# Optimization experiments

Measured on AMD Instinct MI355X. Metric: run time of the kernel, lower is better.

## Reference

```python
import jax, jax.numpy as jnp
import numpy as np

N_NODES = 50000
N_EDGES = 800000
HIDDEN = 128
NUM_RBF = 32
N_GRAPHS = 500
VOCAB = 100


def setup_inputs() -> dict:
    key = jax.random.key(0)
    ks = jax.random.split(key, 16)
    x = jax.random.randint(ks[0], (N_NODES,), 0, VOCAB)
    edge_index = jax.random.randint(ks[1], (2, N_EDGES), 0, N_NODES)
    edge_attr = jax.random.normal(ks[2], (N_EDGES, NUM_RBF), dtype=jnp.float32)
    batch = jnp.sort(jax.random.randint(ks[3], (N_NODES,), 0, N_GRAPHS))
    zdim = 2 * HIDDEN + NUM_RBF
    s = 1.0 / np.sqrt(zdim)
    params = {"emb": jax.random.normal(ks[4], (VOCAB, HIDDEN), dtype=jnp.float32)}
    for l, k0 in zip((1, 2, 3), (5, 8, 11)):
        params[f"Wf{l}"] = jax.random.uniform(ks[k0], (zdim, HIDDEN), minval=-s, maxval=s, dtype=jnp.float32)
        params[f"bf{l}"] = jnp.zeros((HIDDEN,), dtype=jnp.float32)
        params[f"Ws{l}"] = jax.random.uniform(ks[k0 + 1], (zdim, HIDDEN), minval=-s, maxval=s, dtype=jnp.float32)
        params[f"bs{l}"] = jnp.zeros((HIDDEN,), dtype=jnp.float32)
    sl = 1.0 / np.sqrt(HIDDEN)
    params["Wlin"] = jax.random.uniform(ks[14], (HIDDEN, HIDDEN), minval=-sl, maxval=sl, dtype=jnp.float32)
    params["blin"] = jnp.zeros((HIDDEN,), dtype=jnp.float32)
    return {"x": x, "edge_index": edge_index, "edge_attr": edge_attr, "batch": batch, **params}


def _cgconv(h, src, dst, edge_attr, Wf, bf, Ws, bs):
    # z = [x_i || x_j || e_ij]; i = target (dst), j = source (src)
    z = jnp.concatenate([h[dst], h[src], edge_attr], axis=-1)  # [E, 2H+D]
    msg = jax.nn.sigmoid(z @ Wf + bf) * jax.nn.softplus(z @ Ws + bs)  # [E, H]
    agg = jax.ops.segment_sum(msg, dst, num_segments=N_NODES)
    return h + agg


def reference(x, edge_index, edge_attr, batch, emb,
              Wf1, bf1, Ws1, bs1, Wf2, bf2, Ws2, bs2, Wf3, bf3, Ws3, bs3,
              Wlin, blin):
    src, dst = edge_index[0], edge_index[1]
    h = emb[x]  # [N, H]
    h = jax.nn.relu(_cgconv(h, src, dst, edge_attr, Wf1, bf1, Ws1, bs1))
    h = jax.nn.relu(_cgconv(h, src, dst, edge_attr, Wf2, bf2, Ws2, bs2))
    h = jax.nn.relu(_cgconv(h, src, dst, edge_attr, Wf3, bf3, Ws3, bs3))
    sums = jax.ops.segment_sum(h, batch, num_segments=N_GRAPHS)  # [G, H]
    counts = jax.ops.segment_sum(jnp.ones((N_NODES,), h.dtype), batch, num_segments=N_GRAPHS)
    pooled = sums / jnp.maximum(counts, 1.0)[:, None]
    return pooled @ Wlin + blin
```

## Files before the change

### kernel.cpp

```cpp
#include <hip/hip_runtime.h>
#include <hip/hip_bf16.h>
#include <hip/hip_fp16.h>
#include <cstdint>
#include <cstddef>

#define NNODES 50000
#define NEDGES 800000
#define HID 128
#define NRBF 32
#define NGRAPH 500
#define NB_SCAN 196
#define EPB 64
#define NEBLK (NEDGES / EPB)
#define SROWA2 66

typedef __attribute__((ext_vector_type(8))) short short8;
typedef __attribute__((ext_vector_type(4))) float f32x4;

__device__ inline short f2bf(float x) {
  __hip_bfloat16 b = __float2bfloat16(x);
  return *reinterpret_cast<short*>(&b);
}

__device__ inline unsigned int pk_bf16(float a, float b) {
  unsigned int r;
  asm("v_cvt_pk_bf16_f32 %0, %1, %2" : "=v"(r) : "v"(a), "v"(b));
  return r;
}
__device__ inline unsigned int pk_f16(float a, float b) {
  unsigned int r;
  asm("v_cvt_pkrtz_f16_f32 %0, %1, %2" : "=v"(r) : "v"(a), "v"(b));
  return r;
}
__device__ inline unsigned int pk_add_f16(unsigned int a, unsigned int b) {
  unsigned int r;
  asm("v_pk_add_f16 %0, %1, %2" : "=v"(r) : "v"(a), "v"(b));
  return r;
}
__device__ inline float aexp2(float x) {
  float r;
  asm("v_exp_f32 %0, %1" : "=v"(r) : "v"(x));
  return r;
}
__device__ inline float aexp2_nabs(float x) {
  float r;
  asm("v_exp_f32 %0, -abs(%1)" : "=v"(r) : "v"(x));
  return r;
}
__device__ inline float alog2(float x) {
  float r;
  asm("v_log_f32 %0, %1" : "=v"(r) : "v"(x));
  return r;
}

#define SC_F (-1.4426950408889634f)
#define SC_S (1.4426950408889634f)

__global__ void prep_all(
    const float* __restrict__ Wf0, const float* __restrict__ Ws0,
    const float* __restrict__ bf0, const float* __restrict__ bs0,
    const float* __restrict__ Wf1, const float* __restrict__ Ws1,
    const float* __restrict__ bf1, const float* __restrict__ bs1,
    const float* __restrict__ Wf2, const float* __restrict__ Ws2,
    const float* __restrict__ bf2, const float* __restrict__ bs2,
    unsigned short* __restrict__ WtB3, unsigned short* __restrict__ WnB3,
    float* __restrict__ biasv3) {
  const int l = blockIdx.y;
  const float* Wf = (l == 0) ? Wf0 : ((l == 1) ? Wf1 : Wf2);
  const float* Ws = (l == 0) ? Ws0 : ((l == 1) ? Ws1 : Ws2);
  const float* bf = (l == 0) ? bf0 : ((l == 1) ? bf1 : bf2);
  const float* bs = (l == 0) ? bs0 : ((l == 1) ? bs1 : bs2);
  unsigned short* WtB = WtB3 + l * 8192;
  unsigned short* WnB = WnB3 + l * 65536;
  float* biasv = biasv3 + l * 256;

  int i0 = blockIdx.x * blockDim.x + threadIdx.x;
  if (i0 < 8192) {
    int i = i0;
    int j = i & 7, lane = (i >> 3) & 63, t = i >> 9;
    int q = lane >> 4, n = lane & 15;
    int k = q * 8 + j, c = (t & 7) * 16 + n;
    const float* W = (t < 8) ? Wf : Ws;
    const float sc = (t < 8) ? SC_F : SC_S;
    WtB[i] = (unsigned short)f2bf(W[(size_t)(256 + k) * HID + c] * sc);
  } else if (i0 < 8192 + 65536) {
    int i = i0 - 8192;
    int j = i & 7;
    int lane = (i >> 3) & 63;
    int tk = (i >> 9) & 3;
    int tc = i >> 11;
    int q = lane >> 4, n = lane & 15;
    int k = tk * 32 + q * 8 + j;
    float v;
    int which;
    if (tc < 16) {
      int g = tc >> 1;
      which = tc & 1;
      int c = g * 16 + n;
      const float* W = which ? Ws : Wf;
      v = W[(size_t)k * HID + c];
    } else {
      int g = (tc - 16) >> 1;
      which = (tc - 16) & 1;
      int c = g * 16 + n;
      const float* W = which ? Ws : Wf;
      v = W[(size_t)(128 + k) * HID + c];
    }
    WnB[i] = (unsigned short)f2bf(v * (which ? SC_S : SC_F));
    if (i < 256) {
      int c2 = i >> 1, w2 = i & 1;
      biasv[i] = w2 ? bs[c2] * SC_S : bf[c2] * SC_F;
    }
  }
}

__global__ void deg_hist(const int* __restrict__ dst, int* __restrict__ deg) {
  int e = blockIdx.x * blockDim.x + threadIdx.x;
  if (e < NEDGES) atomicAdd(&deg[dst[e]], 1);
}

__global__ __launch_bounds__(256) void scan_block(const int* __restrict__ deg, int* __restrict__ bsum) {
  __shared__ int s[256];
  int i = blockIdx.x * 256 + threadIdx.x;
  s[threadIdx.x] = (i < NNODES) ? deg[i] : 0;
  __syncthreads();
  for (int off = 128; off > 0; off >>= 1) {
    if (threadIdx.x < off) s[threadIdx.x] += s[threadIdx.x + off];
    __syncthreads();
  }
  if (threadIdx.x == 0) bsum[blockIdx.x] = s[0];
}

__global__ __launch_bounds__(256) void scan_top(const int* __restrict__ bsum,
                                                int* __restrict__ bpre) {
  __shared__ int s[256];
  int t = threadIdx.x;
  int v = (t < NB_SCAN) ? bsum[t] : 0;
  s[t] = v;
  __syncthreads();
  for (int off = 1; off < 256; off <<= 1) {
    int u = (t >= off) ? s[t - off] : 0;
    __syncthreads();
    s[t] += u;
    __syncthreads();
  }
  if (t < NB_SCAN) bpre[t] = s[t] - v;
}

__global__ __launch_bounds__(256) void scan_final(const int* __restrict__ deg,
                                                  const int* __restrict__ bpre,
                                                  int* __restrict__ cursor) {
  __shared__ int s[256];
  int i = blockIdx.x * 256 + threadIdx.x;
  int v = (i < NNODES) ? deg[i] : 0;
  s[threadIdx.x] = v;
  __syncthreads();
  for (int off = 1; off < 256; off <<= 1) {
    int t = (threadIdx.x >= off) ? s[threadIdx.x - off] : 0;
    __syncthreads();
    s[threadIdx.x] += t;
    __syncthreads();
  }
  if (i < NNODES) cursor[i] = bpre[blockIdx.x] + s[threadIdx.x] - v;
}

__global__ void scatter_edges_pack(const int* __restrict__ src, const int* __restrict__ dst,
                                   const float* __restrict__ eattr, int* __restrict__ cursor,
                                   int2* __restrict__ se2, unsigned short* __restrict__ eaB) {
  int e = blockIdx.x * blockDim.x + threadIdx.x;
  if (e >= NEDGES) return;
  int d = dst[e];
  int pos = atomicAdd(&cursor[d], 1);
  se2[pos] = make_int2(src[e], d);
  const float* ep = eattr + (size_t)e * NRBF;
  unsigned short* op = eaB + (size_t)pos * NRBF;
#pragma unroll
  for (int part = 0; part < 4; ++part) {
    const float4 v0 = *(const float4*)&ep[part * 8];
    const float4 v1 = *(const float4*)&ep[part * 8 + 4];
    uint4 o;
    o.x = pk_bf16(v0.x, v0.y);
    o.y = pk_bf16(v0.z, v0.w);
    o.z = pk_bf16(v1.x, v1.y);
    o.w = pk_bf16(v1.z, v1.w);
    *(uint4*)&op[part * 8] = o;
  }
}

__global__ __launch_bounds__(256) void node_mfma(
    const int* __restrict__ x, const float* __restrict__ emb,
    float* __restrict__ h, float* __restrict__ agg,
    const unsigned short* __restrict__ WnB, const float* __restrict__ biasv,
    unsigned int* __restrict__ Pdst, unsigned int* __restrict__ Psrc, int mode, int N) {
  const int tid = threadIdx.x;
  const int wv = tid >> 6;
  const int lane = tid & 63;
  const int q = lane >> 4;
  const int n = lane & 15;
  const int nb = blockIdx.x * 32 + (wv >> 1) * 16;
  const int srcwave = wv & 1;
  const int ctile0 = srcwave * 16;

  const bool valid = (nb + n) < N;
  int anode = nb + n;
  if (anode >= N) anode = N - 1;
  float* hp = h + (size_t)anode * HID;

  short8 a[4];
  if (mode == 0) {
    const float* ep = emb + (size_t)x[anode] * HID;
#pragma unroll
    for (int kt = 0; kt < 4; ++kt) {
      const float4 e0 = *(const float4*)&ep[kt * 32 + q * 8];
      const float4 e1 = *(const float4*)&ep[kt * 32 + q * 8 + 4];
      if (valid && !srcwave) {
        *(float4*)&hp[kt * 32 + q * 8] = e0;
        *(float4*)&hp[kt * 32 + q * 8 + 4] = e1;
      }
      union { short8 s8; unsigned int u32[4]; } au;
      au.u32[0] = pk_bf16(e0.x, e0.y);
      au.u32[1] = pk_bf16(e0.z, e0.w);
      au.u32[2] = pk_bf16(e1.x, e1.y);
      au.u32[3] = pk_bf16(e1.z, e1.w);
      a[kt] = au.s8;
    }
  } else {
    float* ap = agg + (size_t)anode * HID;
    float4 ev[8];
#pragma unroll
    for (int kt = 0; kt < 4; ++kt) {
      float4 e0 = *(const float4*)&hp[kt * 32 + q * 8];
      float4 e1 = *(const float4*)&hp[kt * 32 + q * 8 + 4];
      const float4 g0 = *(const float4*)&ap[kt * 32 + q * 8];
      const float4 g1 = *(const float4*)&ap[kt * 32 + q * 8 + 4];
      e0.x = fmaxf(e0.x + g0.x, 0.f); e0.y = fmaxf(e0.y + g0.y, 0.f);
      e0.z = fmaxf(e0.z + g0.z, 0.f); e0.w = fmaxf(e0.w + g0.w, 0.f);
      e1.x = fmaxf(e1.x + g1.x, 0.f); e1.y = fmaxf(e1.y + g1.y, 0.f);
      e1.z = fmaxf(e1.z + g1.z, 0.f); e1.w = fmaxf(e1.w + g1.w, 0.f);
      ev[2 * kt] = e0;
      ev[2 * kt + 1] = e1;
      union { short8 s8; unsigned int u32[4]; } au;
      au.u32[0] = pk_bf16(e0.x, e0.y);
      au.u32[1] = pk_bf16(e0.z, e0.w);
      au.u32[2] = pk_bf16(e1.x, e1.y);
      au.u32[3] = pk_bf16(e1.z, e1.w);
      a[kt] = au.s8;
    }
    __syncthreads();
    if (valid && !srcwave) {
      const float4 z4 = {0.f, 0.f, 0.f, 0.f};
#pragma unroll
      for (int kt = 0; kt < 4; ++kt) {
        *(float4*)&hp[kt * 32 + q * 8] = ev[2 * kt];
        *(float4*)&hp[kt * 32 + q * 8 + 4] = ev[2 * kt + 1];
        *(float4*)&ap[kt * 32 + q * 8] = z4;
        *(float4*)&ap[kt * 32 + q * 8 + 4] = z4;
      }
    }
  }

  const short8* WnB8 = (const short8*)WnB;
  f32x4 acc[16];
#pragma unroll
  for (int tc = 0; tc < 16; ++tc) acc[tc] = (f32x4){0.f, 0.f, 0.f, 0.f};

#pragma unroll
  for (int tc = 0; tc < 16; ++tc) {
#pragma unroll
    for (int kt = 0; kt < 4; ++kt) {
      short8 b = WnB8[((size_t)((ctile0 + tc) * 4 + kt)) * 64 + lane];
      acc[tc] = __builtin_amdgcn_mfma_f32_16x16x32_bf16(a[kt], b, acc[tc], 0, 0, 0);
    }
  }

  if (!srcwave) {
#pragma unroll
    for (int r = 0; r < 4; ++r) {
      const int node = nb + q * 4 + r;
      if (node < N) {
        unsigned int o[8];
#pragma unroll
        for (int g2 = 0; g2 < 8; ++g2) {
          const int c = g2 * 16 + n;
          o[g2] = pk_f16(acc[2 * g2][r] + biasv[2 * c], acc[2 * g2 + 1][r] + biasv[2 * c + 1]);
        }
        *(uint4*)&Pdst[(size_t)node * 128 + n * 8] = make_uint4(o[0], o[1], o[2], o[3]);
        *(uint4*)&Pdst[(size_t)node * 128 + n * 8 + 4] = make_uint4(o[4], o[5], o[6], o[7]);
      }
    }
  } else {
#pragma unroll
    for (int r = 0; r < 4; ++r) {
      const int node = nb + q * 4 + r;
      if (node < N) {
        unsigned int o[8];
#pragma unroll
        for (int g2 = 0; g2 < 8; ++g2) {
          o[g2] = pk_f16(acc[2 * g2][r], acc[2 * g2 + 1][r]);
        }
        *(uint4*)&Psrc[(size_t)node * 128 + n * 8] = make_uint4(o[0], o[1], o[2], o[3]);
        *(uint4*)&Psrc[(size_t)node * 128 + n * 8 + 4] = make_uint4(o[4], o[5], o[6], o[7]);
      }
    }
  }
}

__global__ __launch_bounds__(256) void edge_mfma(
    const unsigned int* __restrict__ Pdst, const unsigned int* __restrict__ Psrc,
    const unsigned short* __restrict__ eaB, const unsigned short* __restrict__ WtB,
    const int2* __restrict__ se2, float* __restrict__ agg) {
  __shared__ unsigned int actL[EPB * SROWA2];
  __shared__ int dstL[EPB];
  __shared__ int grpStart[EPB + 1];
  __shared__ int sndS;

  const int tid = threadIdx.x;
  const int base = blockIdx.x * EPB;
  const int lane = tid & 63;
  const int wv = tid >> 6;
  const int q = lane >> 4;
  const int n = lane & 15;
  const int rowb = wv * 16 + q * 4;

  if (tid < EPB) {
    int2 sd = se2[base + tid];
    dstL[tid] = sd.y;
    int d = sd.y;
    int dprev = __shfl_up(d, 1);
    int flag = (tid == 0 || dprev != d) ? 1 : 0;
    unsigned long long mask = __ballot(flag);
    unsigned long long below = (lane == 63) ? ~0ull : ((1ull << (lane + 1)) - 1);
    int slot = __popcll(mask & below) - 1;
    if (flag) grpStart[slot] = tid;
    if (tid == 0) {
      int nd = __popcll(mask);
      sndS = nd;
      grpStart[nd] = EPB;
    }
  }

  const short8 afrag = *(const short8*)&eaB[(size_t)(base + wv * 16 + n) * 32 + q * 8];

  uint4 spd[8];
#pragma unroll
  for (int r = 0; r < 4; ++r) {
    const int2 sd = se2[base + rowb + r];
    const uint4* ps4 = (const uint4*)(Psrc + (size_t)sd.x * 128 + n * 8);
    const uint4* pd4 = (const uint4*)(Pdst + (size_t)sd.y * 128 + n * 8);
    const uint4 s0 = ps4[0], s1 = ps4[1];
    const uint4 d0 = pd4[0], d1 = pd4[1];
    spd[r * 2].x = pk_add_f16(s0.x, d0.x);
    spd[r * 2].y = pk_add_f16(s0.y, d0.y);
    spd[r * 2].z = pk_add_f16(s0.z, d0.z);
    spd[r * 2].w = pk_add_f16(s0.w, d0.w);
    spd[r * 2 + 1].x = pk_add_f16(s1.x, d1.x);
    spd[r * 2 + 1].y = pk_add_f16(s1.y, d1.y);
    spd[r * 2 + 1].z = pk_add_f16(s1.z, d1.z);
    spd[r * 2 + 1].w = pk_add_f16(s1.w, d1.w);
  }

  const short8* WtB8 = (const short8*)WtB;
  float va[4][4];
#pragma unroll
  for (int t = 0; t < 8; ++t) {
    f32x4 cinf, cins;
#pragma unroll
    for (int r = 0; r < 4; ++r) {
      const uint4 v = spd[r * 2 + (t >> 2)];
      const unsigned int sv = ((t & 3) == 0) ? v.x : ((t & 3) == 1) ? v.y
                             : ((t & 3) == 2) ? v.z : v.w;
      const float2 pz = __half22float2(*reinterpret_cast<const __half2*>(&sv));
      cinf[r] = pz.x;
      cins[r] = pz.y;
    }
    short8 bfr = WtB8[t * 64 + lane];
    short8 bsr = WtB8[(8 + t) * 64 + lane];
    f32x4 cf = __builtin_amdgcn_mfma_f32_16x16x32_bf16(afrag, bfr, cinf, 0, 0, 0);
    f32x4 cs = __builtin_amdgcn_mfma_f32_16x16x32_bf16(afrag, bsr, cins, 0, 0, 0);
#pragma unroll
    for (int r = 0; r < 4; ++r) {
      const float sig = __builtin_amdgcn_rcpf(1.f + aexp2(cf[r]));
      const float sp = fmaxf(cs[r], 0.f) + alog2(1.f + aexp2_nabs(cs[r]));
      const float av = sig * sp;
      if (t < 4) {
        va[t][r] = av;
      } else {
        actL[(rowb + r) * SROWA2 + (t - 4) * 16 + n] = pk_f16(va[t - 4][r], av);
      }
    }
  }
  __syncthreads();

  const int nd = sndS;
  for (int g = wv; g < nd; g += 4) {
    const int jb = grpStart[g];
    const int je = grpStart[g + 1];
    const int d = __builtin_amdgcn_readfirstlane(dstL[jb]);
    float a0 = 0.f, a1 = 0.f;
    unsigned int av_nx = actL[jb * SROWA2 + lane];
    for (int j = jb; j < je; ++j) {
      const unsigned int av = av_nx;
      const int jn = (j + 1 < je) ? (j + 1) : j;
      av_nx = actL[jn * SROWA2 + lane];
      const float2 a2 = __half22float2(*reinterpret_cast<const __half2*>(&av));
      a0 += a2.x;
      a1 += a2.y;
    }
    a0 *= 0.6931471805599453f;
    a1 *= 0.6931471805599453f;
    float* ap0 = agg + (size_t)d * HID + lane;
    float* ap1 = ap0 + 64;
    if (g == 0 || g == nd - 1) {
      atomicAdd(ap0, a0);
      atomicAdd(ap1, a1);
    } else {
      *ap0 = a0;
      *ap1 = a1;
    }
  }
}

__global__ __launch_bounds__(256) void pool_kernel(
    const float* __restrict__ h, const float* __restrict__ agg,
    const int* __restrict__ batch, float* __restrict__ sums, float* __restrict__ counts) {
  __shared__ int gidL[64];
  __shared__ int grpS[65];
  __shared__ int sndP;

  const int tid = threadIdx.x;
  const int lane = tid & 63;
  const int wv = tid >> 6;
  const int nb = blockIdx.x * 64;
  int nvalid = NNODES - nb;
  if (nvalid > 64) nvalid = 64;

  if (tid < 64) {
    int node = nb + tid;
    int g = batch[node < NNODES ? node : NNODES - 1];
    gidL[tid] = g;
    int gprev = __shfl_up(g, 1);
    int flag = (tid < nvalid && (tid == 0 || gprev != g)) ? 1 : 0;
    unsigned long long mask = __ballot(flag);
    int slot = __popcll(mask & ((lane == 63) ? ~0ull : ((1ull << (lane + 1)) - 1))) - 1;
    if (flag) grpS[slot] = tid;
    if (tid == 0) {
      int nd = __popcll(mask);
      sndP = nd;
      grpS[nd] = nvalid;
    }
  }
  __syncthreads();

  const int nd = sndP;
  for (int g = wv; g < nd; g += 4) {
    const int jb = grpS[g];
    const int je = grpS[g + 1];
    const int gid = __builtin_amdgcn_readfirstlane(gidL[jb]);
    float a0 = 0.f, a1 = 0.f;
    for (int j = jb; j < je; ++j) {
      const float2 hv = *(const float2*)&h[(size_t)(nb + j) * HID + 2 * lane];
      const float2 av = *(const float2*)&agg[(size_t)(nb + j) * HID + 2 * lane];
      a0 += fmaxf(hv.x + av.x, 0.f);
      a1 += fmaxf(hv.y + av.y, 0.f);
    }
    float* sp = sums + (size_t)gid * HID + 2 * lane;
    const bool bnd = (g == 0 || g == nd - 1);
    if (bnd) {
      atomicAdd(sp, a0);
      atomicAdd(sp + 1, a1);
    } else {
      *(float2*)sp = make_float2(a0, a1);
    }
    if (lane == 0) {
      if (bnd) atomicAdd(&counts[gid], (float)(je - jb));
      else counts[gid] = (float)(je - jb);
    }
  }
}

__global__ __launch_bounds__(128) void final_kernel(
    const float* __restrict__ sums, const float* __restrict__ counts,
    const float* __restrict__ Wlin, const float* __restrict__ blin,
    float* __restrict__ out) {
  int g = blockIdx.x;
  int c = threadIdx.x;
  __shared__ float pool[HID];
  float cnt = counts[g];
  cnt = cnt > 1.f ? cnt : 1.f;
  pool[c] = sums[(size_t)g * HID + c] / cnt;
  __syncthreads();
  float acc = blin[c];
#pragma unroll 8
  for (int k = 0; k < HID; ++k) acc = fmaf(pool[k], Wlin[k * HID + c], acc);
  out[(size_t)g * HID + c] = acc;
}

extern "C" void kernel_launch(void* const* d_in, const int* in_sizes, int n_in,
                              void* d_out, int out_size, void* d_ws, size_t ws_size,
                              hipStream_t stream) {
  const int* x = (const int*)d_in[0];
  const int* eidx = (const int*)d_in[1];
  const float* eattr = (const float*)d_in[2];
  const int* batch = (const int*)d_in[3];
  const float* emb = (const float*)d_in[4];
  const float* Wf[3] = {(const float*)d_in[5], (const float*)d_in[9], (const float*)d_in[13]};
  const float* bf[3] = {(const float*)d_in[6], (const float*)d_in[10], (const float*)d_in[14]};
  const float* Ws[3] = {(const float*)d_in[7], (const float*)d_in[11], (const float*)d_in[15]};
  const float* bs[3] = {(const float*)d_in[8], (const float*)d_in[12], (const float*)d_in[16]};
  const float* Wlin = (const float*)d_in[17];
  const float* blin = (const float*)d_in[18];
  const int* srcp = eidx;
  const int* dstp = eidx + NEDGES;

  float* wsf = (float*)d_ws;
  float* h = wsf;
  float* PdstF = h + (size_t)NNODES * HID;
  float* agg = PdstF + (size_t)NNODES * 256;
  float* sums = agg + (size_t)NNODES * HID;
  float* counts = sums + (size_t)NGRAPH * HID;
  float* biasv3 = counts + NGRAPH;
  unsigned int* Psrc = (unsigned int*)(biasv3 + 768);
  unsigned short* WtB3 = (unsigned short*)(Psrc + (size_t)NNODES * 128);
  unsigned short* WnB3 = WtB3 + 3 * 8192;
  unsigned short* eaB = WnB3 + 3 * 65536;
  int2* se2 = (int2*)(eaB + (size_t)NEDGES * 32);
  int* deg = (int*)(se2 + NEDGES);
  int* cursor = deg + NNODES;
  int* bsum = cursor + NNODES;
  int* bpre = bsum + NB_SCAN;
  unsigned int* Pdst = (unsigned int*)PdstF;

  dim3 pgrid(288, 3);
  prep_all<<<pgrid, 256, 0, stream>>>(Wf[0], Ws[0], bf[0], bs[0],
                                      Wf[1], Ws[1], bf[1], bs[1],
                                      Wf[2], Ws[2], bf[2], bs[2],
                                      WtB3, WnB3, biasv3);

  hipMemsetAsync(deg, 0, NNODES * sizeof(int), stream);
  deg_hist<<<(NEDGES + 255) / 256, 256, 0, stream>>>(dstp, deg);
  scan_block<<<NB_SCAN, 256, 0, stream>>>(deg, bsum);
  scan_top<<<1, 256, 0, stream>>>(bsum, bpre);
  scan_final<<<NB_SCAN, 256, 0, stream>>>(deg, bpre, cursor);
  scatter_edges_pack<<<(NEDGES + 255) / 256, 256, 0, stream>>>(srcp, dstp, eattr, cursor,
                                                               se2, eaB);

  hipMemsetAsync(agg, 0, (size_t)NNODES * HID * sizeof(float), stream);

  const int nblk_node = (NNODES + 31) / 32;
  for (int l = 0; l < 3; ++l) {
    node_mfma<<<nblk_node, 256, 0, stream>>>(x, emb, h, agg, WnB3 + l * 65536,
                                             biasv3 + l * 256, Pdst, Psrc,
                                             l > 0 ? 1 : 0, NNODES);
    edge_mfma<<<NEBLK, 256, 0, stream>>>(Pdst, Psrc, eaB, WtB3 + l * 8192, se2, agg);
  }

  hipMemsetAsync(sums, 0, (size_t)(NGRAPH * HID + NGRAPH) * sizeof(float), stream);
  pool_kernel<<<(NNODES + 63) / 64, 256, 0, stream>>>(h, agg, batch, sums, counts);
  final_kernel<<<NGRAPH, 128, 0, stream>>>(sums, counts, Wlin, blin, (float*)d_out);
}
```

Before: 706.4 us.

## Store hidden state in fp16 and use per-wave contiguous edge segment reduction

Node hidden features are kept as packed fp16 instead of fp32, halving the read and write traffic for h in the node and pooling kernels. The edge kernel drops the ballot-based group list and has each wave reduce its own 16 consecutive edges, flushing on every destination change and using atomics only for segments crossing wave boundaries. This trades residual precision for bandwidth and may raise atomic counts when destination runs span waves.

```diff
diff --git a/kernel.cpp b/kernel.cpp
--- a/kernel.cpp
+++ b/kernel.cpp
@@ -189,7 +189,7 @@
 
 __global__ __launch_bounds__(256) void node_mfma(
     const int* __restrict__ x, const float* __restrict__ emb,
-    float* __restrict__ h, float* __restrict__ agg,
+    unsigned int* __restrict__ h16, float* __restrict__ agg,
     const unsigned short* __restrict__ WnB, const float* __restrict__ biasv,
     unsigned int* __restrict__ Pdst, unsigned int* __restrict__ Psrc, int mode, int N) {
   const int tid = threadIdx.x;
@@ -204,7 +204,7 @@
   const bool valid = (nb + n) < N;
   int anode = nb + n;
   if (anode >= N) anode = N - 1;
-  float* hp = h + (size_t)anode * HID;
+  unsigned int* hp = h16 + (size_t)anode * 64;
 
   short8 a[4];
   if (mode == 0) {
@@ -214,8 +214,12 @@
       const float4 e0 = *(const float4*)&ep[kt * 32 + q * 8];
       const float4 e1 = *(const float4*)&ep[kt * 32 + q * 8 + 4];
       if (valid && !srcwave) {
-        *(float4*)&hp[kt * 32 + q * 8] = e0;
-        *(float4*)&hp[kt * 32 + q * 8 + 4] = e1;
+        uint4 hv;
+        hv.x = pk_f16(e0.x, e0.y);
+        hv.y = pk_f16(e0.z, e0.w);
+        hv.z = pk_f16(e1.x, e1.y);
+        hv.w = pk_f16(e1.z, e1.w);
+        *(uint4*)&hp[kt * 16 + q * 4] = hv;
       }
       union { short8 s8; unsigned int u32[4]; } au;
       au.u32[0] = pk_bf16(e0.x, e0.y);
@@ -226,24 +230,33 @@
     }
   } else {
     float* ap = agg + (size_t)anode * HID;
-    float4 ev[8];
+    uint4 hnew[4];
 #pragma unroll
     for (int kt = 0; kt < 4; ++kt) {
-      float4 e0 = *(const float4*)&hp[kt * 32 + q * 8];
-      float4 e1 = *(const float4*)&hp[kt * 32 + q * 8 + 4];
+      const uint4 hv = *(const uint4*)&hp[kt * 16 + q * 4];
+      const float2 h0 = __half22float2(*reinterpret_cast<const __half2*>(&hv.x));
+      const float2 h1 = __half22float2(*reinterpret_cast<const __half2*>(&hv.y));
+      const float2 h2 = __half22float2(*reinterpret_cast<const __half2*>(&hv.z));
+      const float2 h3 = __half22float2(*reinterpret_cast<const __half2*>(&hv.w));
       const float4 g0 = *(const float4*)&ap[kt * 32 + q * 8];
       const float4 g1 = *(const float4*)&ap[kt * 32 + q * 8 + 4];
-      e0.x = fmaxf(e0.x + g0.x, 0.f); e0.y = fmaxf(e0.y + g0.y, 0.f);
-      e0.z = fmaxf(e0.z + g0.z, 0.f); e0.w = fmaxf(e0.w + g0.w, 0.f);
-      e1.x = fmaxf(e1.x + g1.x, 0.f); e1.y = fmaxf(e1.y + g1.y, 0.f);
-      e1.z = fmaxf(e1.z + g1.z, 0.f); e1.w = fmaxf(e1.w + g1.w, 0.f);
-      ev[2 * kt] = e0;
-      ev[2 * kt + 1] = e1;
+      const float e0 = fmaxf(h0.x + g0.x, 0.f);
+      const float e1 = fmaxf(h0.y + g0.y, 0.f);
+      const float e2 = fmaxf(h1.x + g0.z, 0.f);
+      const float e3 = fmaxf(h1.y + g0.w, 0.f);
+      const float e4 = fmaxf(h2.x + g1.x, 0.f);
+      const float e5 = fmaxf(h2.y + g1.y, 0.f);
+      const float e6 = fmaxf(h3.x + g1.z, 0.f);
+      const float e7 = fmaxf(h3.y + g1.w, 0.f);
+      hnew[kt].x = pk_f16(e0, e1);
+      hnew[kt].y = pk_f16(e2, e3);
+      hnew[kt].z = pk_f16(e4, e5);
+      hnew[kt].w = pk_f16(e6, e7);
       union { short8 s8; unsigned int u32[4]; } au;
-      au.u32[0] = pk_bf16(e0.x, e0.y);
-      au.u32[1] = pk_bf16(e0.z, e0.w);
-      au.u32[2] = pk_bf16(e1.x, e1.y);
-      au.u32[3] = pk_bf16(e1.z, e1.w);
+      au.u32[0] = pk_bf16(e0, e1);
+      au.u32[1] = pk_bf16(e2, e3);
+      au.u32[2] = pk_bf16(e4, e5);
+      au.u32[3] = pk_bf16(e6, e7);
       a[kt] = au.s8;
     }
     __syncthreads();
@@ -251,8 +264,7 @@
       const float4 z4 = {0.f, 0.f, 0.f, 0.f};
 #pragma unroll
       for (int kt = 0; kt < 4; ++kt) {
-        *(float4*)&hp[kt * 32 + q * 8] = ev[2 * kt];
-        *(float4*)&hp[kt * 32 + q * 8 + 4] = ev[2 * kt + 1];
+        *(uint4*)&hp[kt * 16 + q * 4] = hnew[kt];
         *(float4*)&ap[kt * 32 + q * 8] = z4;
         *(float4*)&ap[kt * 32 + q * 8 + 4] = z4;
       }
@@ -311,8 +323,6 @@
     const int2* __restrict__ se2, float* __restrict__ agg) {
   __shared__ unsigned int actL[EPB * SROWA2];
   __shared__ int dstL[EPB];
-  __shared__ int grpStart[EPB + 1];
-  __shared__ int sndS;
 
   const int tid = threadIdx.x;
   const int base = blockIdx.x * EPB;
@@ -322,22 +332,7 @@
   const int n = lane & 15;
   const int rowb = wv * 16 + q * 4;
 
-  if (tid < EPB) {
-    int2 sd = se2[base + tid];
-    dstL[tid] = sd.y;
-    int d = sd.y;
-    int dprev = __shfl_up(d, 1);
-    int flag = (tid == 0 || dprev != d) ? 1 : 0;
-    unsigned long long mask = __ballot(flag);
-    unsigned long long below = (lane == 63) ? ~0ull : ((1ull << (lane + 1)) - 1);
-    int slot = __popcll(mask & below) - 1;
-    if (flag) grpStart[slot] = tid;
-    if (tid == 0) {
-      int nd = __popcll(mask);
-      sndS = nd;
-      grpStart[nd] = EPB;
-    }
-  }
+  if (tid < EPB) dstL[tid] = se2[base + tid].y;
 
   const short8 afrag = *(const short8*)&eaB[(size_t)(base + wv * 16 + n) * 32 + q * 8];
 
@@ -391,37 +386,56 @@
   }
   __syncthreads();
 
-  const int nd = sndS;
-  for (int g = wv; g < nd; g += 4) {
-    const int jb = grpStart[g];
-    const int je = grpStart[g + 1];
-    const int d = __builtin_amdgcn_readfirstlane(dstL[jb]);
-    float a0 = 0.f, a1 = 0.f;
-    unsigned int av_nx = actL[jb * SROWA2 + lane];
-    for (int j = jb; j < je; ++j) {
-      const unsigned int av = av_nx;
-      const int jn = (j + 1 < je) ? (j + 1) : j;
-      av_nx = actL[jn * SROWA2 + lane];
-      const float2 a2 = __half22float2(*reinterpret_cast<const __half2*>(&av));
-      a0 += a2.x;
-      a1 += a2.y;
-    }
-    a0 *= 0.6931471805599453f;
-    a1 *= 0.6931471805599453f;
+  const int j0 = wv * 16;
+  const int j1 = j0 + 16;
+  int dcur = dstL[j0];
+  bool openL = (j0 == 0) || (dstL[j0 - 1] == dcur);
+  float a0 = 0.f, a1 = 0.f;
+  unsigned int av_nx = actL[j0 * SROWA2 + lane];
+  for (int j = j0; j < j1; ++j) {
+    const int dj = dstL[j];
+    if (dj != dcur) {
+      const int d = __builtin_amdgcn_readfirstlane(dcur);
+      float* ap0 = agg + (size_t)d * HID + lane;
+      const float f0 = a0 * 0.6931471805599453f;
+      const float f1 = a1 * 0.6931471805599453f;
+      if (openL) {
+        atomicAdd(ap0, f0);
+        atomicAdd(ap0 + 64, f1);
+      } else {
+        ap0[0] = f0;
+        ap0[64] = f1;
+      }
+      dcur = dj;
+      openL = false;
+      a0 = 0.f;
+      a1 = 0.f;
+    }
+    const unsigned int av = av_nx;
+    const int jn = (j + 1 < j1) ? (j + 1) : j;
+    av_nx = actL[jn * SROWA2 + lane];
+    const float2 a2 = __half22float2(*reinterpret_cast<const __half2*>(&av));
+    a0 += a2.x;
+    a1 += a2.y;
+  }
+  {
+    const bool openR = (j1 == EPB) || (dstL[j1] == dcur);
+    const int d = __builtin_amdgcn_readfirstlane(dcur);
     float* ap0 = agg + (size_t)d * HID + lane;
-    float* ap1 = ap0 + 64;
-    if (g == 0 || g == nd - 1) {
-      atomicAdd(ap0, a0);
-      atomicAdd(ap1, a1);
+    const float f0 = a0 * 0.6931471805599453f;
+    const float f1 = a1 * 0.6931471805599453f;
+    if (openL || openR) {
+      atomicAdd(ap0, f0);
+      atomicAdd(ap0 + 64, f1);
     } else {
-      *ap0 = a0;
-      *ap1 = a1;
+      ap0[0] = f0;
+      ap0[64] = f1;
     }
   }
 }
 
 __global__ __launch_bounds__(256) void pool_kernel(
-    const float* __restrict__ h, const float* __restrict__ agg,
+    const unsigned int* __restrict__ h16, const float* __restrict__ agg,
     const int* __restrict__ batch, float* __restrict__ sums, float* __restrict__ counts) {
   __shared__ int gidL[64];
   __shared__ int grpS[65];
@@ -458,10 +472,11 @@
     const int gid = __builtin_amdgcn_readfirstlane(gidL[jb]);
     float a0 = 0.f, a1 = 0.f;
     for (int j = jb; j < je; ++j) {
-      const float2 hv = *(const float2*)&h[(size_t)(nb + j) * HID + 2 * lane];
+      const unsigned int hv = h16[(size_t)(nb + j) * 64 + lane];
+      const float2 hf = __half22float2(*reinterpret_cast<const __half2*>(&hv));
       const float2 av = *(const float2*)&agg[(size_t)(nb + j) * HID + 2 * lane];
-      a0 += fmaxf(hv.x + av.x, 0.f);
-      a1 += fmaxf(hv.y + av.y, 0.f);
+      a0 += fmaxf(hf.x + av.x, 0.f);
+      a1 += fmaxf(hf.y + av.y, 0.f);
     }
     float* sp = sums + (size_t)gid * HID + 2 * lane;
     const bool bnd = (g == 0 || g == nd - 1);
@@ -513,8 +528,8 @@
   const int* dstp = eidx + NEDGES;
 
   float* wsf = (float*)d_ws;
-  float* h = wsf;
-  float* PdstF = h + (size_t)NNODES * HID;
+  float* hF = wsf;
+  float* PdstF = hF + (size_t)NNODES * HID;
   float* agg = PdstF + (size_t)NNODES * 256;
   float* sums = agg + (size_t)NNODES * HID;
   float* counts = sums + (size_t)NGRAPH * HID;
@@ -529,6 +544,7 @@
   int* bsum = cursor + NNODES;
   int* bpre = bsum + NB_SCAN;
   unsigned int* Pdst = (unsigned int*)PdstF;
+  unsigned int* h16 = (unsigned int*)hF;
 
   dim3 pgrid(288, 3);
   prep_all<<<pgrid, 256, 0, stream>>>(Wf[0], Ws[0], bf[0], bs[0],
@@ -548,13 +564,13 @@
 
   const int nblk_node = (NNODES + 31) / 32;
   for (int l = 0; l < 3; ++l) {
-    node_mfma<<<nblk_node, 256, 0, stream>>>(x, emb, h, agg, WnB3 + l * 65536,
+    node_mfma<<<nblk_node, 256, 0, stream>>>(x, emb, h16, agg, WnB3 + l * 65536,
                                              biasv3 + l * 256, Pdst, Psrc,
                                              l > 0 ? 1 : 0, NNODES);
     edge_mfma<<<NEBLK, 256, 0, stream>>>(Pdst, Psrc, eaB, WtB3 + l * 8192, se2, agg);
   }
 
   hipMemsetAsync(sums, 0, (size_t)(NGRAPH * HID + NGRAPH) * sizeof(float), stream);
-  pool_kernel<<<(NNODES + 63) / 64, 256, 0, stream>>>(h, agg, batch, sums, counts);
+  pool_kernel<<<(NNODES + 63) / 64, 256, 0, stream>>>(h16, agg, batch, sums, counts);
   final_kernel<<<NGRAPH, 128, 0, stream>>>(sums, counts, Wlin, blin, (float*)d_out);
 }
```

Result: no change. 709.8 us (+0.5%).
